# Performance work log

Hardware: AMD Instinct MI355X
Metric: run time of the kernel (lower is better)

The kernel has to match this reference:

```python
import jax, jax.numpy as jnp
import numpy as np

H = 8          # num_heads
D = 32         # out_feats per head
E = 500_000    # number of metapath instances (edges)
N = 100_000    # number of destination nodes
NEG_SLOPE = 0.01


def setup_inputs() -> dict:
    key = jax.random.key(0)
    k1, k2, k3 = jax.random.split(key, 3)
    feat0 = jax.random.normal(k1, (E, H * D), dtype=jnp.float32)
    # learned parameter attn_r [1, H, D] (xavier_normal in torch; plain normal suffices)
    attn_r = jax.random.normal(k2, (1, H, D), dtype=jnp.float32) * 0.1
    dst_idx = jax.random.randint(k3, (E,), 0, N)
    return {"feat0": feat0, "attn_r": attn_r, "dst_idx": dst_idx, "num_dst": N}


def reference(feat0, attn_r, dst_idx, num_dst):
    # [E, H, D] per-head metapath-instance features (feat_drop is identity in eval)
    h = feat0.reshape(-1, H, D)
    # er = sum(h * attn_r) over feature dim -> [E, H]
    er = jnp.sum(h * attn_r, axis=-1)
    # leaky relu on edge scores
    e = jnp.where(er > 0, er, NEG_SLOPE * er)
    # per-destination-node edge softmax (stable: subtract segment max)
    emax = jax.lax.stop_gradient(
        jax.ops.segment_max(e, dst_idx, num_segments=num_dst))  # [N, H]
    num = jnp.exp(e - emax[dst_idx])                            # [E, H]
    den = jax.ops.segment_sum(num, dst_idx, num_segments=num_dst)  # [N, H]
    a = num / den[dst_idx]                                      # [E, H]
    # attention-weighted scatter-sum aggregation: sum_e a_e * h_e per dst node
    m = h * a[..., None]                                        # [E, H, D]
    out = jax.ops.segment_sum(m, dst_idx, num_segments=num_dst)  # [N, H, D]
    # ELU activation then flatten heads
    out = jnp.where(out > 0, out, jnp.expm1(out))
    return out.reshape(num_dst, H * D)
```

## Files before the change

kernel.cpp:

```cpp
#include <hip/hip_runtime.h>
#include <hip/hip_bf16.h>

#define H 8
#define D 32
#define HD 256
#define NEG_SLOPE 0.01f

typedef float f32x4 __attribute__((ext_vector_type(4)));


__global__ void hist_kernel(const int* __restrict__ dst, int E, int* __restrict__ count) {
    int i = blockIdx.x * blockDim.x + threadIdx.x;
    int base = i * 4;
    if (base + 3 < E) {
        int4 d = *reinterpret_cast<const int4*>(dst + base);
        atomicAdd(&count[d.x], 1);
        atomicAdd(&count[d.y], 1);
        atomicAdd(&count[d.z], 1);
        atomicAdd(&count[d.w], 1);
    } else {
        for (int k = base; k < E; ++k) atomicAdd(&count[dst[k]], 1);
    }
}

__global__ void scan_block_kernel(const int* __restrict__ in, int n,
                                  int* __restrict__ out_excl, int* __restrict__ bsum) {
    __shared__ int s[256];
    int t = threadIdx.x;
    int i = blockIdx.x * 256 + t;
    int v = (i < n) ? in[i] : 0;
    s[t] = v;
    __syncthreads();
    for (int off = 1; off < 256; off <<= 1) {
        int x = (t >= off) ? s[t - off] : 0;
        __syncthreads();
        s[t] += x;
        __syncthreads();
    }
    if (i < n) out_excl[i] = s[t] - v;
    if (t == 255) bsum[blockIdx.x] = s[255];
}

__global__ void add_base_kernel(const int* __restrict__ off_excl,
                                const int* __restrict__ count,
                                const int* __restrict__ bsum, int nb, int n,
                                int2* __restrict__ pack, int* __restrict__ cursor) {
    __shared__ int s[512];
    int t = threadIdx.x;
    s[t] = (t < nb) ? bsum[t] : 0;
    s[t + 256] = (t + 256 < nb) ? bsum[t + 256] : 0;
    __syncthreads();
    for (int off = 1; off < 512; off <<= 1) {
        int x0 = (t >= off) ? s[t - off] : 0;
        int x1 = (t + 256 >= off) ? s[t + 256 - off] : 0;
        __syncthreads();
        s[t] += x0;
        s[t + 256] += x1;
        __syncthreads();
    }
    int b = blockIdx.x;
    int base = (b > 0) ? s[b - 1] : 0;
    int i = b * 256 + t;
    if (i < n) {
        int o = off_excl[i] + base;
        pack[i] = make_int2(o, count[i]);
        cursor[i] = o;
    }
}

__global__ void scatter_kernel(const int* __restrict__ dst, int E,
                               int* __restrict__ cursor, int* __restrict__ csr) {
    int i = blockIdx.x * blockDim.x + threadIdx.x;
    int base = i * 4;
    if (base + 3 < E) {
        int4 d = *reinterpret_cast<const int4*>(dst + base);
        int p0 = atomicAdd(&cursor[d.x], 1); csr[p0] = base;
        int p1 = atomicAdd(&cursor[d.y], 1); csr[p1] = base + 1;
        int p2 = atomicAdd(&cursor[d.z], 1); csr[p2] = base + 2;
        int p3 = atomicAdd(&cursor[d.w], 1); csr[p3] = base + 3;
    } else {
        for (int k = base; k < E; ++k) {
            int p = atomicAdd(&cursor[dst[k]], 1);
            csr[p] = k;
        }
    }
}

__global__ void aggregate_kernel(const float* __restrict__ feat,
                                 const float* __restrict__ attn_r,
                                 const int* __restrict__ csr,
                                 const int2* __restrict__ pack,
                                 float* __restrict__ out, int N) {
    int gtid = blockIdx.x * blockDim.x + threadIdx.x;
    int node = gtid >> 6;
    int lane = threadIdx.x & 63;
    if (node >= N) return;

    f32x4 ar = reinterpret_cast<const f32x4*>(attn_r)[lane];
    int2 se  = pack[node];
    int start = se.x;
    int len   = se.y;

    f32x4 acc = (f32x4)(0.f);
    float den = 0.f;

    const f32x4* featv = reinterpret_cast<const f32x4*>(feat);

#define LOADF(i, fi) if (r > (i)) { int e = __shfl(eidx, c + (i)); \
    fi = __builtin_nontemporal_load(&featv[(size_t)e * 64 + lane]); }
#define PROC(fi) { \
    float part = fi.x * ar.x + fi.y * ar.y + fi.z * ar.z + fi.w * ar.w; \
    part += __shfl_xor(part, 1); \
    part += __shfl_xor(part, 2); \
    part += __shfl_xor(part, 4); \
    float el  = (part > 0.f) ? part : NEG_SLOPE * part; \
    float num = __expf(el); \
    den   += num; \
    acc.x += num * fi.x; acc.y += num * fi.y; \
    acc.z += num * fi.z; acc.w += num * fi.w; }

    for (int base = 0; base < len; base += 64) {
        int rem = min(64, len - base);
        int eidx = csr[start + base + min(lane, rem - 1)];

        for (int c = 0; c < rem; c += 8) {
            int r = rem - c;
            f32x4 f0, f1, f2, f3, f4, f5, f6, f7;
            { int e = __shfl(eidx, c); f0 = __builtin_nontemporal_load(&featv[(size_t)e * 64 + lane]); }
            LOADF(1, f1) LOADF(2, f2) LOADF(3, f3)
            LOADF(4, f4) LOADF(5, f5) LOADF(6, f6) LOADF(7, f7)
            PROC(f0)
            if (r > 1) PROC(f1)
            if (r > 2) PROC(f2)
            if (r > 3) PROC(f3)
            if (r > 4) PROC(f4)
            if (r > 5) PROC(f5)
            if (r > 6) PROC(f6)
            if (r > 7) PROC(f7)
        }
    }
#undef LOADF
#undef PROC

    float inv = (len > 0) ? (1.0f / den) : 0.0f;
    f32x4 o;
    o.x = acc.x * inv;
    o.y = acc.y * inv;
    o.z = acc.z * inv;
    o.w = acc.w * inv;
    o.x = (o.x > 0.f) ? o.x : expm1f(o.x);
    o.y = (o.y > 0.f) ? o.y : expm1f(o.y);
    o.z = (o.z > 0.f) ? o.z : expm1f(o.z);
    o.w = (o.w > 0.f) ? o.w : expm1f(o.w);
    __builtin_nontemporal_store(o, &reinterpret_cast<f32x4*>(out)[(size_t)node * 64 + lane]);
}


extern "C" void kernel_launch(void* const* d_in, const int* in_sizes, int n_in,
                              void* d_out, int out_size, void* d_ws, size_t ws_size,
                              hipStream_t stream) {
    const float* feat   = (const float*)d_in[0];
    const float* attn_r = (const float*)d_in[1];
    const int*   dst    = (const int*)d_in[2];
    float*       out    = (float*)d_out;

    const int E = in_sizes[0] / HD;
    const int N = out_size / HD;
    const int NB = (N + 255) / 256;

    int*  count    = (int*)d_ws;
    int*  off_excl = count + N;
    int*  cursor   = off_excl + N;
    int*  bsum     = cursor + N;
    int2* pack     = (int2*)(bsum + 512);
    int*  csr      = (int*)(pack + N);

    (void)hipMemsetAsync(count, 0, (size_t)N * sizeof(int), stream);

    const int E4 = (E + 3) / 4;
    hist_kernel<<<(E4 + 255) / 256, 256, 0, stream>>>(dst, E, count);
    scan_block_kernel<<<NB, 256, 0, stream>>>(count, N, off_excl, bsum);
    add_base_kernel<<<NB, 256, 0, stream>>>(off_excl, count, bsum, NB, N, pack, cursor);
    scatter_kernel<<<(E4 + 255) / 256, 256, 0, stream>>>(dst, E, cursor, csr);

    aggregate_kernel<<<(N + 3) / 4, 256, 0, stream>>>(feat, attn_r, csr, pack, out, N);
}
```

Measured before the change: 170.3 us.

## Process two nodes per wave and merge scan kernels via atomic block allocation

The two-pass prefix scan (block scan plus base add) is replaced by a single kernel in which each block claims its output range with an atomicAdd on a global cursor. CSR segments therefore stay contiguous per node but are no longer ordered by node. The aggregate kernel now assigns two destination nodes to each 64-lane wave, interleaving their gather loads to raise memory-level parallelism for short segments (average degree is about 5). Degrees above 32 fall back to a serial loop, and an extra workspace counter must be zeroed.

```diff
diff --git a/kernel.cpp b/kernel.cpp
--- a/kernel.cpp
+++ b/kernel.cpp
@@ -23,12 +23,14 @@
     }
 }
 
-__global__ void scan_block_kernel(const int* __restrict__ in, int n,
-                                  int* __restrict__ out_excl, int* __restrict__ bsum) {
+__global__ void scan_alloc_kernel(const int* __restrict__ count, int n,
+                                  int* __restrict__ gcursor,
+                                  int2* __restrict__ pack, int* __restrict__ cursor) {
     __shared__ int s[256];
+    __shared__ int base_s;
     int t = threadIdx.x;
     int i = blockIdx.x * 256 + t;
-    int v = (i < n) ? in[i] : 0;
+    int v = (i < n) ? count[i] : 0;
     s[t] = v;
     __syncthreads();
     for (int off = 1; off < 256; off <<= 1) {
@@ -37,34 +39,12 @@
         s[t] += x;
         __syncthreads();
     }
-    if (i < n) out_excl[i] = s[t] - v;
-    if (t == 255) bsum[blockIdx.x] = s[255];
-}
-
-__global__ void add_base_kernel(const int* __restrict__ off_excl,
-                                const int* __restrict__ count,
-                                const int* __restrict__ bsum, int nb, int n,
-                                int2* __restrict__ pack, int* __restrict__ cursor) {
-    __shared__ int s[512];
-    int t = threadIdx.x;
-    s[t] = (t < nb) ? bsum[t] : 0;
-    s[t + 256] = (t + 256 < nb) ? bsum[t + 256] : 0;
+    if (t == 255) base_s = atomicAdd(gcursor, s[255]);
     __syncthreads();
-    for (int off = 1; off < 512; off <<= 1) {
-        int x0 = (t >= off) ? s[t - off] : 0;
-        int x1 = (t + 256 >= off) ? s[t + 256 - off] : 0;
-        __syncthreads();
-        s[t] += x0;
-        s[t + 256] += x1;
-        __syncthreads();
-    }
-    int b = blockIdx.x;
-    int base = (b > 0) ? s[b - 1] : 0;
-    int i = b * 256 + t;
     if (i < n) {
-        int o = off_excl[i] + base;
-        pack[i] = make_int2(o, count[i]);
-        cursor[i] = o;
+        int start = base_s + s[t] - v;
+        pack[i] = make_int2(start, v);
+        cursor[i] = start;
     }
 }
 
@@ -90,69 +70,91 @@
                                  const float* __restrict__ attn_r,
                                  const int* __restrict__ csr,
                                  const int2* __restrict__ pack,
-                                 float* __restrict__ out, int N) {
-    int gtid = blockIdx.x * blockDim.x + threadIdx.x;
-    int node = gtid >> 6;
+                                 float* __restrict__ out, int N, int E) {
+    int wid  = (blockIdx.x * blockDim.x + threadIdx.x) >> 6;
     int lane = threadIdx.x & 63;
-    if (node >= N) return;
+    int nA = wid * 2;
+    int nB = nA + 1;
+    if (nA >= N) return;
 
     f32x4 ar = reinterpret_cast<const f32x4*>(attn_r)[lane];
-    int2 se  = pack[node];
-    int start = se.x;
-    int len   = se.y;
 
-    f32x4 acc = (f32x4)(0.f);
-    float den = 0.f;
+    int4 se = reinterpret_cast<const int4*>(pack)[wid];
+    int startA = se.x, lenA = se.y;
+    int startB = se.z, lenB = se.w;
+    if (nB >= N) { startB = 0; lenB = 0; }
+
+    int half  = lane >> 5;
+    int hl    = lane & 31;
+    int st_h  = half ? startB : startA;
+    int ln_h  = half ? lenB   : lenA;
+    int off_h = (ln_h > 0) ? min(hl, ln_h - 1) : 0;
+    int eidx  = csr[min(st_h + off_h, E - 1)];
+
+    f32x4 accA = (f32x4)(0.f), accB = (f32x4)(0.f);
+    float denA = 0.f, denB = 0.f;
 
     const f32x4* featv = reinterpret_cast<const f32x4*>(feat);
 
-#define LOADF(i, fi) if (r > (i)) { int e = __shfl(eidx, c + (i)); \
-    fi = __builtin_nontemporal_load(&featv[(size_t)e * 64 + lane]); }
-#define PROC(fi) { \
+#define PROC(fi, accX, denX) { \
     float part = fi.x * ar.x + fi.y * ar.y + fi.z * ar.z + fi.w * ar.w; \
     part += __shfl_xor(part, 1); \
     part += __shfl_xor(part, 2); \
     part += __shfl_xor(part, 4); \
     float el  = (part > 0.f) ? part : NEG_SLOPE * part; \
     float num = __expf(el); \
-    den   += num; \
-    acc.x += num * fi.x; acc.y += num * fi.y; \
-    acc.z += num * fi.z; acc.w += num * fi.w; }
+    denX += num; \
+    accX.x += num * fi.x; accX.y += num * fi.y; \
+    accX.z += num * fi.z; accX.w += num * fi.w; }
 
-    for (int base = 0; base < len; base += 64) {
-        int rem = min(64, len - base);
-        int eidx = csr[start + base + min(lane, rem - 1)];
+    int lenC = min(max(lenA, lenB), 32);
+    for (int c = 0; c < lenC; c += 4) {
+        f32x4 a0, a1, a2, a3, b0, b1, b2, b3;
+        if (lenA > c    ) { int e = __shfl(eidx, c    ); a0 = __builtin_nontemporal_load(&featv[(size_t)e * 64 + lane]); }
+        if (lenA > c + 1) { int e = __shfl(eidx, c + 1); a1 = __builtin_nontemporal_load(&featv[(size_t)e * 64 + lane]); }
+        if (lenA > c + 2) { int e = __shfl(eidx, c + 2); a2 = __builtin_nontemporal_load(&featv[(size_t)e * 64 + lane]); }
+        if (lenA > c + 3) { int e = __shfl(eidx, c + 3); a3 = __builtin_nontemporal_load(&featv[(size_t)e * 64 + lane]); }
+        if (lenB > c    ) { int e = __shfl(eidx, 32 + c    ); b0 = __builtin_nontemporal_load(&featv[(size_t)e * 64 + lane]); }
+        if (lenB > c + 1) { int e = __shfl(eidx, 32 + c + 1); b1 = __builtin_nontemporal_load(&featv[(size_t)e * 64 + lane]); }
+        if (lenB > c + 2) { int e = __shfl(eidx, 32 + c + 2); b2 = __builtin_nontemporal_load(&featv[(size_t)e * 64 + lane]); }
+        if (lenB > c + 3) { int e = __shfl(eidx, 32 + c + 3); b3 = __builtin_nontemporal_load(&featv[(size_t)e * 64 + lane]); }
+        if (lenA > c    ) PROC(a0, accA, denA)
+        if (lenA > c + 1) PROC(a1, accA, denA)
+        if (lenA > c + 2) PROC(a2, accA, denA)
+        if (lenA > c + 3) PROC(a3, accA, denA)
+        if (lenB > c    ) PROC(b0, accB, denB)
+        if (lenB > c + 1) PROC(b1, accB, denB)
+        if (lenB > c + 2) PROC(b2, accB, denB)
+        if (lenB > c + 3) PROC(b3, accB, denB)
+    }
 
-        for (int c = 0; c < rem; c += 8) {
-            int r = rem - c;
-            f32x4 f0, f1, f2, f3, f4, f5, f6, f7;
-            { int e = __shfl(eidx, c); f0 = __builtin_nontemporal_load(&featv[(size_t)e * 64 + lane]); }
-            LOADF(1, f1) LOADF(2, f2) LOADF(3, f3)
-            LOADF(4, f4) LOADF(5, f5) LOADF(6, f6) LOADF(7, f7)
-            PROC(f0)
-            if (r > 1) PROC(f1)
-            if (r > 2) PROC(f2)
-            if (r > 3) PROC(f3)
-            if (r > 4) PROC(f4)
-            if (r > 5) PROC(f5)
-            if (r > 6) PROC(f6)
-            if (r > 7) PROC(f7)
-        }
+    for (int k = 32; k < lenA; ++k) {
+        int e = csr[startA + k];
+        f32x4 f = __builtin_nontemporal_load(&featv[(size_t)e * 64 + lane]);
+        PROC(f, accA, denA)
     }
-#undef LOADF
+    for (int k = 32; k < lenB; ++k) {
+        int e = csr[startB + k];
+        f32x4 f = __builtin_nontemporal_load(&featv[(size_t)e * 64 + lane]);
+        PROC(f, accB, denB)
+    }
 #undef PROC
 
-    float inv = (len > 0) ? (1.0f / den) : 0.0f;
-    f32x4 o;
-    o.x = acc.x * inv;
-    o.y = acc.y * inv;
-    o.z = acc.z * inv;
-    o.w = acc.w * inv;
-    o.x = (o.x > 0.f) ? o.x : expm1f(o.x);
-    o.y = (o.y > 0.f) ? o.y : expm1f(o.y);
-    o.z = (o.z > 0.f) ? o.z : expm1f(o.z);
-    o.w = (o.w > 0.f) ? o.w : expm1f(o.w);
-    __builtin_nontemporal_store(o, &reinterpret_cast<f32x4*>(out)[(size_t)node * 64 + lane]);
+#define FINISH(accX, denX, node) { \
+    float inv = ((node) < N && denX > 0.f) ? (1.0f / denX) : 0.0f; \
+    f32x4 o; \
+    o.x = accX.x * inv; o.y = accX.y * inv; \
+    o.z = accX.z * inv; o.w = accX.w * inv; \
+    o.x = (o.x > 0.f) ? o.x : expm1f(o.x); \
+    o.y = (o.y > 0.f) ? o.y : expm1f(o.y); \
+    o.z = (o.z > 0.f) ? o.z : expm1f(o.z); \
+    o.w = (o.w > 0.f) ? o.w : expm1f(o.w); \
+    if ((node) < N) \
+        __builtin_nontemporal_store(o, &reinterpret_cast<f32x4*>(out)[(size_t)(node) * 64 + lane]); }
+
+    FINISH(accA, denA, nA)
+    FINISH(accB, denB, nB)
+#undef FINISH
 }
 
 
@@ -168,20 +170,20 @@
     const int N = out_size / HD;
     const int NB = (N + 255) / 256;
 
-    int*  count    = (int*)d_ws;
-    int*  off_excl = count + N;
-    int*  cursor   = off_excl + N;
-    int*  bsum     = cursor + N;
-    int2* pack     = (int2*)(bsum + 512);
-    int*  csr      = (int*)(pack + N);
+    int2* pack    = (int2*)d_ws;
+    int*  count   = (int*)(pack + (N + 2));
+    int*  gcursor = count + N;
+    int*  cursor  = gcursor + 1;
+    int*  csr     = cursor + N;
 
-    (void)hipMemsetAsync(count, 0, (size_t)N * sizeof(int), stream);
+    (void)hipMemsetAsync(count, 0, (size_t)(N + 1) * sizeof(int), stream);
 
     const int E4 = (E + 3) / 4;
     hist_kernel<<<(E4 + 255) / 256, 256, 0, stream>>>(dst, E, count);
-    scan_block_kernel<<<NB, 256, 0, stream>>>(count, N, off_excl, bsum);
-    add_base_kernel<<<NB, 256, 0, stream>>>(off_excl, count, bsum, NB, N, pack, cursor);
+    scan_alloc_kernel<<<NB, 256, 0, stream>>>(count, N, gcursor, pack, cursor);
     scatter_kernel<<<(E4 + 255) / 256, 256, 0, stream>>>(dst, E, cursor, csr);
 
-    aggregate_kernel<<<(N + 3) / 4, 256, 0, stream>>>(feat, attn_r, csr, pack, out, N);
+    const int nwaves = (N + 1) / 2;
+    const int nblocks = (nwaves + 3) / 4;
+    aggregate_kernel<<<nblocks, 256, 0, stream>>>(feat, attn_r, csr, pack, out, N, E);
 }
```

New measurement: 183.8 us. 7.9% more time.

## Fuse scan passes via atomic bucket allocation and shrink aggregate blocks

Applied to the files above, without the earlier changes.

Replaces the two-kernel exact prefix scan with a single kernel in which each block reserves its CSR range by an atomicAdd on a global cursor, so bucket order across blocks is arbitrary but every node still gets a contiguous range. This removes one launch and the second scan pass. The aggregate kernel now runs 128-thread blocks of two waves, and each block fetches both nodes' (start,len) pairs with one int4 load. The pack buffer is padded by two entries so that load stays in bounds for an odd N.

```diff
diff --git a/kernel.cpp b/kernel.cpp
--- a/kernel.cpp
+++ b/kernel.cpp
@@ -23,12 +23,14 @@
     }
 }
 
-__global__ void scan_block_kernel(const int* __restrict__ in, int n,
-                                  int* __restrict__ out_excl, int* __restrict__ bsum) {
+__global__ void scan_alloc_kernel(const int* __restrict__ count, int n,
+                                  int* __restrict__ gcursor,
+                                  int2* __restrict__ pack, int* __restrict__ cursor) {
     __shared__ int s[256];
+    __shared__ int base_s;
     int t = threadIdx.x;
     int i = blockIdx.x * 256 + t;
-    int v = (i < n) ? in[i] : 0;
+    int v = (i < n) ? count[i] : 0;
     s[t] = v;
     __syncthreads();
     for (int off = 1; off < 256; off <<= 1) {
@@ -37,34 +39,12 @@
         s[t] += x;
         __syncthreads();
     }
-    if (i < n) out_excl[i] = s[t] - v;
-    if (t == 255) bsum[blockIdx.x] = s[255];
-}
-
-__global__ void add_base_kernel(const int* __restrict__ off_excl,
-                                const int* __restrict__ count,
-                                const int* __restrict__ bsum, int nb, int n,
-                                int2* __restrict__ pack, int* __restrict__ cursor) {
-    __shared__ int s[512];
-    int t = threadIdx.x;
-    s[t] = (t < nb) ? bsum[t] : 0;
-    s[t + 256] = (t + 256 < nb) ? bsum[t + 256] : 0;
+    if (t == 255) base_s = atomicAdd(gcursor, s[255]);
     __syncthreads();
-    for (int off = 1; off < 512; off <<= 1) {
-        int x0 = (t >= off) ? s[t - off] : 0;
-        int x1 = (t + 256 >= off) ? s[t + 256 - off] : 0;
-        __syncthreads();
-        s[t] += x0;
-        s[t + 256] += x1;
-        __syncthreads();
-    }
-    int b = blockIdx.x;
-    int base = (b > 0) ? s[b - 1] : 0;
-    int i = b * 256 + t;
     if (i < n) {
-        int o = off_excl[i] + base;
-        pack[i] = make_int2(o, count[i]);
-        cursor[i] = o;
+        int start = base_s + s[t] - v;
+        pack[i] = make_int2(start, v);
+        cursor[i] = start;
     }
 }
 
@@ -91,15 +71,17 @@
                                  const int* __restrict__ csr,
                                  const int2* __restrict__ pack,
                                  float* __restrict__ out, int N) {
-    int gtid = blockIdx.x * blockDim.x + threadIdx.x;
-    int node = gtid >> 6;
+    int b    = blockIdx.x;
+    int w    = threadIdx.x >> 6;
     int lane = threadIdx.x & 63;
+    int node = b * 2 + w;
+
+    int4 se = reinterpret_cast<const int4*>(pack)[b];
+    int start = w ? se.z : se.x;
+    int len   = w ? se.w : se.y;
     if (node >= N) return;
 
     f32x4 ar = reinterpret_cast<const f32x4*>(attn_r)[lane];
-    int2 se  = pack[node];
-    int start = se.x;
-    int len   = se.y;
 
     f32x4 acc = (f32x4)(0.f);
     float den = 0.f;
@@ -168,20 +150,19 @@
     const int N = out_size / HD;
     const int NB = (N + 255) / 256;
 
-    int*  count    = (int*)d_ws;
-    int*  off_excl = count + N;
-    int*  cursor   = off_excl + N;
-    int*  bsum     = cursor + N;
-    int2* pack     = (int2*)(bsum + 512);
-    int*  csr      = (int*)(pack + N);
+    int2* pack    = (int2*)d_ws;
+    int*  count   = (int*)(pack + (N + 2));
+    int*  gcursor = count + N;
+    int*  cursor  = gcursor + 1;
+    int*  csr     = cursor + N;
 
-    (void)hipMemsetAsync(count, 0, (size_t)N * sizeof(int), stream);
+    (void)hipMemsetAsync(count, 0, (size_t)(N + 1) * sizeof(int), stream);
 
     const int E4 = (E + 3) / 4;
     hist_kernel<<<(E4 + 255) / 256, 256, 0, stream>>>(dst, E, count);
-    scan_block_kernel<<<NB, 256, 0, stream>>>(count, N, off_excl, bsum);
-    add_base_kernel<<<NB, 256, 0, stream>>>(off_excl, count, bsum, NB, N, pack, cursor);
+    scan_alloc_kernel<<<NB, 256, 0, stream>>>(count, N, gcursor, pack, cursor);
     scatter_kernel<<<(E4 + 255) / 256, 256, 0, stream>>>(dst, E, cursor, csr);
 
-    aggregate_kernel<<<(N + 3) / 4, 256, 0, stream>>>(feat, attn_r, csr, pack, out, N);
+    const int nblocks = (N + 1) / 2;
+    aggregate_kernel<<<nblocks, 128, 0, stream>>>(feat, attn_r, csr, pack, out, N);
 }
```

Result: no change. 173.1 us (+1.6%).
